# Performance work log

Hardware: AMD Instinct MI355X
Metric: run time of the kernel (lower is better)

Reference implementation:

```python
import jax, jax.numpy as jnp
import numpy as np

B, N, F_IN = 8, 4096, 32
NRP = 1024
D_MODEL = 512
K = 64  # max_num_neighbors
STAGE_CFG = ((1024, 0.05), (256, 0.3), (64, 0.5))  # (num_samples=ceil(0.25*N_in), radius)


def fps(pos, m):
    """Farthest point sampling of m points from pos (N,3), deterministic start at 0."""
    d = jnp.sum((pos - pos[0]) ** 2, axis=-1)
    idxs = jnp.zeros((m,), jnp.int32)
    def body(i, carry):
        idxs, d = carry
        nxt = jnp.argmax(d).astype(jnp.int32)
        d = jnp.minimum(d, jnp.sum((pos - pos[nxt]) ** 2, axis=-1))
        return (idxs.at[i].set(nxt), d)
    idxs, _ = jax.lax.fori_loop(1, m, body, (idxs, d))
    return idxs


def apply_mlp(h, ws, bs):
    for w, b in zip(ws[:-1], bs[:-1]):
        h = jax.nn.relu(h @ w + b)
    return h @ ws[-1] + bs[-1]


def sa_stage(x, pos, m, r, ws, bs):
    """SAModule: FPS -> radius neighbors (<=K) -> PointNetConv (gather, MLP, max-scatter)."""
    idx = jax.vmap(lambda p: fps(p, m))(pos)                          # (B,m)
    pos_s = jnp.take_along_axis(pos, idx[..., None], axis=1)          # (B,m,3)
    d2 = jnp.sum((pos_s[:, :, None, :] - pos[:, None, :, :]) ** 2, -1)  # (B,m,N)
    neg = jnp.where(d2 <= r * r, -d2, -jnp.inf)
    vals, nbr = jax.lax.top_k(neg, K)                                 # (B,m,K) nearest within r
    valid = vals > -jnp.inf                                           # self always valid (d2=0)
    x_j = jax.vmap(lambda xb, nb: xb[nb])(x, nbr)                     # (B,m,K,F) gather
    p_j = jax.vmap(lambda pb, nb: pb[nb])(pos, nbr)                   # (B,m,K,3)
    h = jnp.concatenate([x_j, p_j - pos_s[:, :, None, :]], axis=-1)   # message input
    h = apply_mlp(h, ws, bs)
    h = jnp.where(valid[..., None], h, -jnp.inf)
    return jnp.max(h, axis=2), pos_s                                  # max aggregation


def _forward(point_cloud_features, point_cloud, emb_table, point_id_emb, stage_params):
    x = emb_table[point_cloud_features[..., 0]]                       # (B,N,F_IN)
    x = x.at[:, :NRP].add(point_id_emb)
    pos = point_cloud
    for (m, r), (ws, bs) in zip(STAGE_CFG, stage_params):
        x, pos = sa_stage(x, pos, m, r, ws, bs)
    return x, pos                                                     # (B,64,D_MODEL), (B,64,3)


def setup_inputs() -> dict:
    key = jax.random.key(0)
    ks = iter(jax.random.split(key, 64))
    def nrm(shape, s=0.05):
        return s * jax.random.normal(next(ks), shape, dtype=jnp.float32)
    inp = {
        "point_cloud_features": jax.random.randint(next(ks), (B, N, 1), 0, 3),
        "point_cloud": jax.random.uniform(next(ks), (B, N, 3), dtype=jnp.float32),
        "emb_table": nrm((3, F_IN), 1.0),
        "point_id_emb": nrm((1, NRP, F_IN), 1.0),
    }
    dims = {"s1": [3 + F_IN, 64, 64, 64], "s2": [64 + 3, 128, 128, 256], "s3": [256 + 3, 256, 512, D_MODEL]}
    for s, d in dims.items():
        for i in range(3):
            inp[f"{s}w{i}"] = nrm((d[i], d[i + 1]))
            inp[f"{s}b{i}"] = jnp.zeros((d[i + 1],), jnp.float32)
    return inp


def reference(point_cloud_features, point_cloud, emb_table, point_id_emb,
              s1w0, s1b0, s1w1, s1b1, s1w2, s1b2,
              s2w0, s2b0, s2w1, s2b1, s2w2, s2b2,
              s3w0, s3b0, s3w1, s3b1, s3w2, s3b2):
    stage_params = [
        ([s1w0, s1w1, s1w2], [s1b0, s1b1, s1b2]),
        ([s2w0, s2w1, s2w2], [s2b0, s2b1, s2b2]),
        ([s3w0, s3w1, s3w2], [s3b0, s3b1, s3b2]),
    ]
    return _forward(point_cloud_features, point_cloud, emb_table, point_id_emb, stage_params)
```

## Files before the change

kernel.cpp:

```cpp
#include <hip/hip_runtime.h>

#define DEVI static __device__ __forceinline__

constexpr int B = 8;
constexpr int N0 = 4096;
constexpr int KNB = 64;

typedef float f32x2 __attribute__((ext_vector_type(2)));
typedef float f32x4 __attribute__((ext_vector_type(4)));
typedef short bf16x8 __attribute__((ext_vector_type(8)));

DEVI float dist2f(float ax, float ay, float az, float bx, float by, float bz) {
#pragma clang fp contract(off)
  float dx = ax - bx;
  float dy = ay - by;
  float dz = az - bz;
  return (dx * dx + dy * dy) + dz * dz;
}
DEVI f32x2 dist2v(f32x2 ax, f32x2 ay, f32x2 az, float bx, float by, float bz) {
#pragma clang fp contract(off)
  f32x2 dx = ax - bx;
  f32x2 dy = ay - by;
  f32x2 dz = az - bz;
  return (dx * dx + dy * dy) + dz * dz;
}

DEVI unsigned long long packMinKey(float v, int i) {
  return ((unsigned long long)__float_as_uint(v) << 32) | (unsigned int)i;
}

template <int CTRL, int RM>
DEVI unsigned long long dppMaxU64(unsigned long long k) {
  unsigned lo = (unsigned)k, hi = (unsigned)(k >> 32);
  unsigned mlo = (unsigned)__builtin_amdgcn_update_dpp((int)lo, (int)lo, CTRL, RM, 0xf, false);
  unsigned mhi = (unsigned)__builtin_amdgcn_update_dpp((int)hi, (int)hi, CTRL, RM, 0xf, false);
  unsigned long long o = ((unsigned long long)mhi << 32) | mlo;
  return (k > o) ? k : o;
}
DEVI unsigned long long waveReduceMaxU64(unsigned long long k) {
  k = dppMaxU64<0x111, 0xf>(k);
  k = dppMaxU64<0x112, 0xf>(k);
  k = dppMaxU64<0x114, 0xf>(k);
  k = dppMaxU64<0x118, 0xf>(k);
  k = dppMaxU64<0x142, 0xa>(k);
  k = dppMaxU64<0x143, 0xc>(k);
  unsigned lo = (unsigned)__builtin_amdgcn_readlane((int)(unsigned)k, 63);
  unsigned hi = (unsigned)__builtin_amdgcn_readlane((int)(unsigned)(k >> 32), 63);
  return ((unsigned long long)hi << 32) | lo;
}

DEVI unsigned short bfhi(float x) {
  unsigned u = __float_as_uint(x);
  return (unsigned short)((u + 0x7FFFu + ((u >> 16) & 1u)) >> 16);
}
DEVI float bf2f(unsigned short h) { return __uint_as_float(((unsigned)h) << 16); }
DEVI void mkfrag(const float* p, bf16x8& hi, bf16x8& lo) {
#pragma unroll
  for (int e = 0; e < 8; ++e) {
    float x = p[e];
    unsigned short h = bfhi(x);
    float r = x - bf2f(h);
    unsigned short l2 = bfhi(r);
    hi[e] = (short)h;
    lo[e] = (short)l2;
  }
}


DEVI void x0_body(const int* __restrict__ feat, const float* __restrict__ emb,
                  const float* __restrict__ pid, float* __restrict__ x0buf,
                  int bx, int t) {
  int gid = bx * 256 + t;
  if (gid >= B * N0 * 32) return;
  int c = gid & 31;
  int bn = gid >> 5;
  int n = bn & (N0 - 1);
  int f = feat[bn];
  float v = emb[f * 32 + c];
  if (n < 1024) v += pid[n * 32 + c];
  x0buf[gid] = v;
}

DEVI void pack_body(int gid, const float* __restrict__ W, int Kreal, int KS,
                    int N, unsigned short* __restrict__ hi,
                    unsigned short* __restrict__ lo) {
  int e = gid & 7;
  int l = (gid >> 3) & 63;
  int rest = gid >> 9;
  int ks = rest % KS;
  int nt = rest / KS;
  int n = nt * 16 + (l & 15);
  int k = ks * 32 + (l >> 4) * 8 + e;
  float val = (k < Kreal) ? W[(size_t)k * N + n] : 0.f;
  unsigned short h = bfhi(val);
  float r = val - bf2f(h);
  hi[gid] = h;
  lo[gid] = bfhi(r);
}

template <int NPTS, int M, int BLK>
DEVI void fps_body(char* smem, const float* __restrict__ pos,
                   float* __restrict__ pos_out, int b, int t) {
  constexpr int EPT = NPTS / BLK;
  constexpr int EP2 = EPT / 2;
  constexpr int NW = BLK / 64;
  float4* posl = (float4*)smem;
  float4* outp = (float4*)(smem + (size_t)NPTS * 16);
  unsigned long long* redk =
      (unsigned long long*)(smem + (size_t)(NPTS + M) * 16);
  const float* pb = pos + (size_t)b * NPTS * 3;
  f32x2 px[EP2], py[EP2], pz[EP2], d[EP2];
#pragma unroll
  for (int e = 0; e < EP2; ++e) {
    int i0 = t + (2 * e) * BLK;
    int i1 = t + (2 * e + 1) * BLK;
    float x0 = pb[i0 * 3 + 0], y0 = pb[i0 * 3 + 1], z0 = pb[i0 * 3 + 2];
    float x1 = pb[i1 * 3 + 0], y1 = pb[i1 * 3 + 1], z1 = pb[i1 * 3 + 2];
    px[e] = (f32x2){x0, x1};
    py[e] = (f32x2){y0, y1};
    pz[e] = (f32x2){z0, z1};
    posl[i0] = make_float4(x0, y0, z0, 0.f);
    posl[i1] = make_float4(x1, y1, z1, 0.f);
  }
  float sx = pb[0], sy = pb[1], sz = pb[2];
  if (t == 0) outp[0] = make_float4(sx, sy, sz, 0.f);
  f32x2 m2 = (f32x2){-1.f, -1.f};
#pragma unroll
  for (int e = 0; e < EP2; ++e) {
    d[e] = dist2v(px[e], py[e], pz[e], sx, sy, sz);
    m2.x = fmaxf(m2.x, d[e].x);
    m2.y = fmaxf(m2.y, d[e].y);
  }
  for (int it = 1; it < M; ++it) {
    const float lm = fmaxf(m2.x, m2.y);
    unsigned cand = 0xffffffffu;
#pragma unroll
    for (int e = 0; e < EP2; ++e) {
      unsigned c0 = (d[e].x == lm) ? (unsigned)(t + (2 * e) * BLK) : 0xffffffffu;
      unsigned c1 = (d[e].y == lm) ? (unsigned)(t + (2 * e + 1) * BLK) : 0xffffffffu;
      unsigned cc = c0 < c1 ? c0 : c1;
      cand = cand < cc ? cand : cc;
    }
    unsigned long long k =
        ((unsigned long long)__float_as_uint(lm) << 32) |
        (unsigned)(0x7fffffffu - cand);
    k = waveReduceMaxU64(k);
    unsigned sel;
    if constexpr (NW > 1) {
      if ((t & 63) == 0) redk[(it & 1) * NW + (t >> 6)] = k;
      __syncthreads();
      unsigned long long kk = redk[(it & 1) * NW + 0];
#pragma unroll
      for (int w = 1; w < NW; ++w) {
        unsigned long long o = redk[(it & 1) * NW + w];
        kk = (kk > o) ? kk : o;
      }
      sel = 0x7fffffffu - (unsigned)(kk & 0xffffffffULL);
    } else {
      sel = 0x7fffffffu - (unsigned)(k & 0xffffffffULL);
    }
    float4 sp = posl[sel];
    if (t == 0) outp[it] = sp;
    f32x2 mm = (f32x2){-1.f, -1.f};
#pragma unroll
    for (int e = 0; e < EP2; ++e) {
      f32x2 nd = dist2v(px[e], py[e], pz[e], sp.x, sp.y, sp.z);
      d[e].x = fminf(d[e].x, nd.x);
      d[e].y = fminf(d[e].y, nd.y);
      mm.x = fmaxf(mm.x, d[e].x);
      mm.y = fmaxf(mm.y, d[e].y);
    }
    m2 = mm;
  }
  if constexpr (NW > 1) __syncthreads();
  for (int m = t; m < M; m += BLK) {
    float4 q = outp[m];
    pos_out[(size_t)(b * M + m) * 3 + 0] = q.x;
    pos_out[(size_t)(b * M + m) * 3 + 1] = q.y;
    pos_out[(size_t)(b * M + m) * 3 + 2] = q.z;
  }
}

template <int NPTS, int M>
DEVI void radius_body(char* smem, const float* __restrict__ pos,
                      const float* __restrict__ pos_s, float r2,
                      int* __restrict__ nbr, int* __restrict__ cnt, int blk,
                      int t) {
  unsigned long long* candkey = (unsigned long long*)smem;
  int* ctrp = (int*)(smem + (size_t)NPTS * 8);
  const int b = blk / M;
  const float* pb = pos + (size_t)b * NPTS * 3;
  const float cx = pos_s[(size_t)blk * 3 + 0];
  const float cy = pos_s[(size_t)blk * 3 + 1];
  const float cz = pos_s[(size_t)blk * 3 + 2];
  if (t == 0) *ctrp = 0;
  __syncthreads();
  for (int j = t; j < NPTS; j += 256) {
    float d2 = dist2f(pb[j * 3 + 0], pb[j * 3 + 1], pb[j * 3 + 2], cx, cy, cz);
    if (d2 <= r2) {
      int p = atomicAdd(ctrp, 1);
      candkey[p] = packMinKey(d2, j);
      if (p < KNB) nbr[(size_t)blk * KNB + p] = j;
    }
  }
  __syncthreads();
  const int c = *ctrp;
  if (c <= KNB) {
    if (t == 0) cnt[blk] = c;
    return;
  }
  for (int s = t; s < c; s += 256) {
    unsigned long long mykey = candkey[s];
    int rank = 0;
#pragma unroll 4
    for (int j = 0; j < c; ++j) {
      rank += (candkey[j] < mykey) ? 1 : 0;
    }
    if (rank < KNB)
      nbr[(size_t)blk * KNB + rank] = (int)(unsigned)(mykey & 0xffffffffULL);
  }
  if (t == 0) cnt[blk] = KNB;
}

DEVI void conv1_body(char* smem, const float* __restrict__ x0buf,
                     const float* __restrict__ pos,
                     const float* __restrict__ pos_s,
                     const int* __restrict__ nbr, const int* __restrict__ cntp,
                     const float* __restrict__ w0, const float* __restrict__ b0,
                     const float* __restrict__ w1, const float* __restrict__ b1,
                     const float* __restrict__ w2, const float* __restrict__ b2,
                     float* __restrict__ x1, int blk, int t) {
  float(*ins)[36] = (float(*)[36])smem;
  float(*hh)[65] = (float(*)[65])(smem + 576);
  float(*sred)[65] = (float(*)[65])(smem + 1616);
  const int slot = t >> 6;
  const int ch = t & 63;
  const int b = blk >> 10;
  const int c = cntp[blk];
  const float cx = pos_s[(size_t)blk * 3 + 0];
  const float cy = pos_s[(size_t)blk * 3 + 1];
  const float cz = pos_s[(size_t)blk * 3 + 2];
  float best = -__builtin_inff();
  for (int r0 = 0; r0 < c; r0 += 4) {
    const int r = r0 + slot;
    const bool act = r < c;
    const int j = nbr[(size_t)blk * KNB + (act ? r : 0)];
    if (ch < 32) {
      ins[slot][ch] = x0buf[((size_t)(b * N0) + j) * 32 + ch];
    } else if (ch < 35) {
      float pv = pos[((size_t)(b * N0) + j) * 3 + (ch - 32)];
      float cv = (ch == 32) ? cx : (ch == 33) ? cy : cz;
      ins[slot][ch] = pv - cv;
    }
    __syncthreads();
    float v = b0[ch];
#pragma unroll
    for (int i = 0; i < 35; ++i) v = fmaf(ins[slot][i], w0[i * 64 + ch], v);
    v = fmaxf(v, 0.f);
    hh[slot][ch] = v;
    __syncthreads();
    float v2 = b1[ch];
#pragma unroll
    for (int i = 0; i < 64; ++i) v2 = fmaf(hh[slot][i], w1[i * 64 + ch], v2);
    v2 = fmaxf(v2, 0.f);
    __syncthreads();
    hh[slot][ch] = v2;
    __syncthreads();
    float v3 = b2[ch];
#pragma unroll
    for (int i = 0; i < 64; ++i) v3 = fmaf(hh[slot][i], w2[i * 64 + ch], v3);
    if (act) best = fmaxf(best, v3);
    __syncthreads();
  }
  sred[slot][ch] = best;
  __syncthreads();
  if (t < 64) {
    float v = sred[0][t];
#pragma unroll
    for (int s = 1; s < 4; ++s) v = fmaxf(v, sred[s][t]);
    x1[(size_t)blk * 64 + t] = v;
  }
}

DEVI void conv2_mfma_body(char* smem, const float* __restrict__ x1,
                          const float* __restrict__ pos1,
                          const float* __restrict__ pos2,
                          const int* __restrict__ nbr,
                          const int* __restrict__ cntp,
                          const unsigned short* __restrict__ w0h,
                          const float* __restrict__ b0,
                          const unsigned short* __restrict__ w1h,
                          const float* __restrict__ b1,
                          const unsigned short* __restrict__ w2h,
                          const float* __restrict__ b2,
                          float* __restrict__ x2, int blk, int t) {
  float(*h1)[132] = (float(*)[132])smem;
  float(*h2)[132] = (float(*)[132])(smem + 33792);
  float* red = (float*)smem;
  const int b = blk >> 8;
  const int c = cntp[blk];
  const int w = t >> 6;
  const int lane = t & 63;
  const int cb = lane & 15;
  const int kb = lane >> 4;
  const int mrow = w * 16 + cb;
  const int jrow = nbr[(size_t)blk * KNB + (mrow < c ? mrow : c - 1)];
  const float* xrow = x1 + ((size_t)(b * 1024) + jrow) * 64;
  const float cx = pos2[(size_t)blk * 3 + 0];
  const float cy = pos2[(size_t)blk * 3 + 1];
  const float cz = pos2[(size_t)blk * 3 + 2];

  f32x4 acc1[8];
#pragma unroll
  for (int nt = 0; nt < 8; ++nt) acc1[nt] = (f32x4){0.f, 0.f, 0.f, 0.f};
#pragma unroll
  for (int ks = 0; ks < 2; ++ks) {
    float xv[8];
    *(float4*)&xv[0] = *(const float4*)&xrow[ks * 32 + kb * 8];
    *(float4*)&xv[4] = *(const float4*)&xrow[ks * 32 + kb * 8 + 4];
    bf16x8 ahi, alo;
    mkfrag(xv, ahi, alo);
#pragma unroll
    for (int nt = 0; nt < 8; ++nt) {
      size_t off = ((size_t)(nt * 3 + ks) * 64 + lane) * 8;
      bf16x8 bhi = *(const bf16x8*)(w0h + off);
      acc1[nt] = __builtin_amdgcn_mfma_f32_16x16x32_bf16(ahi, bhi, acc1[nt], 0, 0, 0);
      acc1[nt] = __builtin_amdgcn_mfma_f32_16x16x32_bf16(alo, bhi, acc1[nt], 0, 0, 0);
    }
  }
  {
    float xv[8] = {0.f, 0.f, 0.f, 0.f, 0.f, 0.f, 0.f, 0.f};
    if (kb == 0) {
      xv[0] = pos1[((size_t)(b * 1024) + jrow) * 3 + 0] - cx;
      xv[1] = pos1[((size_t)(b * 1024) + jrow) * 3 + 1] - cy;
      xv[2] = pos1[((size_t)(b * 1024) + jrow) * 3 + 2] - cz;
    }
    bf16x8 ahi, alo;
    mkfrag(xv, ahi, alo);
#pragma unroll
    for (int nt = 0; nt < 8; ++nt) {
      size_t off = ((size_t)(nt * 3 + 2) * 64 + lane) * 8;
      bf16x8 bhi = *(const bf16x8*)(w0h + off);
      acc1[nt] = __builtin_amdgcn_mfma_f32_16x16x32_bf16(ahi, bhi, acc1[nt], 0, 0, 0);
      acc1[nt] = __builtin_amdgcn_mfma_f32_16x16x32_bf16(alo, bhi, acc1[nt], 0, 0, 0);
    }
  }
  {
    const int mw = w * 16 + kb * 4;
#pragma unroll
    for (int nt = 0; nt < 8; ++nt) {
      float bias = b0[nt * 16 + cb];
#pragma unroll
      for (int r = 0; r < 4; ++r)
        h1[mw + r][nt * 16 + cb] = fmaxf(acc1[nt][r] + bias, 0.f);
    }
  }

  f32x4 acc2[8];
#pragma unroll
  for (int nt = 0; nt < 8; ++nt) acc2[nt] = (f32x4){0.f, 0.f, 0.f, 0.f};
#pragma unroll
  for (int ks = 0; ks < 4; ++ks) {
    bf16x8 ahi, alo;
    mkfrag(&h1[mrow][ks * 32 + kb * 8], ahi, alo);
#pragma unroll
    for (int nt = 0; nt < 8; ++nt) {
      size_t off = ((size_t)(nt * 4 + ks) * 64 + lane) * 8;
      bf16x8 bhi = *(const bf16x8*)(w1h + off);
      acc2[nt] = __builtin_amdgcn_mfma_f32_16x16x32_bf16(ahi, bhi, acc2[nt], 0, 0, 0);
      acc2[nt] = __builtin_amdgcn_mfma_f32_16x16x32_bf16(alo, bhi, acc2[nt], 0, 0, 0);
    }
  }
  {
    const int mw = w * 16 + kb * 4;
#pragma unroll
    for (int nt = 0; nt < 8; ++nt) {
      float bias = b1[nt * 16 + cb];
#pragma unroll
      for (int r = 0; r < 4; ++r)
        h2[mw + r][nt * 16 + cb] = fmaxf(acc2[nt][r] + bias, 0.f);
    }
  }

  f32x4 acc3[16];
#pragma unroll
  for (int nt = 0; nt < 16; ++nt) acc3[nt] = (f32x4){0.f, 0.f, 0.f, 0.f};
#pragma unroll
  for (int ks = 0; ks < 4; ++ks) {
    bf16x8 ahi, alo;
    mkfrag(&h2[mrow][ks * 32 + kb * 8], ahi, alo);
#pragma unroll
    for (int nt = 0; nt < 16; ++nt) {
      size_t off = ((size_t)(nt * 4 + ks) * 64 + lane) * 8;
      bf16x8 bhi = *(const bf16x8*)(w2h + off);
      acc3[nt] = __builtin_amdgcn_mfma_f32_16x16x32_bf16(ahi, bhi, acc3[nt], 0, 0, 0);
      acc3[nt] = __builtin_amdgcn_mfma_f32_16x16x32_bf16(alo, bhi, acc3[nt], 0, 0, 0);
    }
  }
  __syncthreads();
  {
    const int mw = w * 16 + kb * 4;
#pragma unroll
    for (int nt = 0; nt < 16; ++nt) {
      float bias = b2[nt * 16 + cb];
      float mx = -__builtin_inff();
#pragma unroll
      for (int r = 0; r < 4; ++r) {
        if (mw + r < c) mx = fmaxf(mx, acc3[nt][r] + bias);
      }
      red[(w * 4 + kb) * 256 + nt * 16 + cb] = mx;
    }
  }
  __syncthreads();
  {
    float v = red[t];
#pragma unroll
    for (int g = 1; g < 16; ++g) v = fmaxf(v, red[g * 256 + t]);
    x2[(size_t)blk * 256 + t] = v;
  }
}


constexpr int PK_T0 = 16 * 9 * 64 * 8;
constexpr int PK_T1 = 32 * 8 * 64 * 8;
constexpr int PK_T2 = 32 * 16 * 64 * 8;
constexpr int PK_U0 = 8 * 3 * 64 * 8;
constexpr int PK_U1 = 8 * 4 * 64 * 8;
constexpr int PK_U2 = 16 * 4 * 64 * 8;
constexpr int PK_TOTAL = PK_T0 + PK_T1 + PK_T2 + PK_U0 + PK_U1 + PK_U2;
constexpr int PK_BLOCKS = PK_TOTAL / 256;

__global__ void __launch_bounds__(256) l1_kernel(
    const float* __restrict__ pos, float* __restrict__ pos1,
    const int* __restrict__ feat, const float* __restrict__ emb,
    const float* __restrict__ pid, float* __restrict__ x0buf,
    const float* __restrict__ s3w0, const float* __restrict__ s3w1,
    const float* __restrict__ s3w2, const float* __restrict__ s2w0,
    const float* __restrict__ s2w1, const float* __restrict__ s2w2,
    unsigned short* __restrict__ w0h, unsigned short* __restrict__ w0l,
    unsigned short* __restrict__ w1h, unsigned short* __restrict__ w1l,
    unsigned short* __restrict__ w2h, unsigned short* __restrict__ w2l,
    unsigned short* __restrict__ v0h, unsigned short* __restrict__ v0l,
    unsigned short* __restrict__ v1h, unsigned short* __restrict__ v1l,
    unsigned short* __restrict__ v2h, unsigned short* __restrict__ v2l) {
  __shared__ __attribute__((aligned(16))) char smem[81984];
  int bx = blockIdx.x;
  if (bx < 8) {
    fps_body<4096, 1024, 256>(smem, pos, pos1, bx, threadIdx.x);
    return;
  }
  bx -= 8;
  if (bx < 4096) {
    x0_body(feat, emb, pid, x0buf, bx, threadIdx.x);
    return;
  }
  bx -= 4096;
  int gid = bx * 256 + threadIdx.x;
  if (gid < PK_T0) { pack_body(gid, s3w0, 259, 9, 256, w0h, w0l); return; }
  gid -= PK_T0;
  if (gid < PK_T1) { pack_body(gid, s3w1, 256, 8, 512, w1h, w1l); return; }
  gid -= PK_T1;
  if (gid < PK_T2) { pack_body(gid, s3w2, 512, 16, 512, w2h, w2l); return; }
  gid -= PK_T2;
  if (gid < PK_U0) { pack_body(gid, s2w0, 67, 3, 128, v0h, v0l); return; }
  gid -= PK_U0;
  if (gid < PK_U1) { pack_body(gid, s2w1, 128, 4, 128, v1h, v1l); return; }
  gid -= PK_U1;
  if (gid < PK_U2) { pack_body(gid, s2w2, 128, 4, 256, v2h, v2l); return; }
}

__global__ void __launch_bounds__(256) l2_kernel(
    const float* __restrict__ pos1, float* __restrict__ pos2,
    const float* __restrict__ pos, float r2a, int* __restrict__ nbr1,
    int* __restrict__ cnt1) {
  __shared__ __attribute__((aligned(16))) char smem[33024];
  if (blockIdx.x < 8) {
    if (threadIdx.x < 64)
      fps_body<1024, 256, 64>(smem, pos1, pos2, blockIdx.x, threadIdx.x);
  } else {
    radius_body<4096, 1024>(smem, pos, pos1, r2a, nbr1, cnt1, blockIdx.x - 8,
                            threadIdx.x);
  }
}

__global__ void __launch_bounds__(256) l3_kernel(
    const float* __restrict__ pos2, float* __restrict__ pos3, float r2b,
    int* __restrict__ nbr2, int* __restrict__ cnt2,
    const float* __restrict__ pos1, const float* __restrict__ x0buf,
    const float* __restrict__ pos, const int* __restrict__ nbr1,
    const int* __restrict__ cnt1, const float* __restrict__ w0,
    const float* __restrict__ b0, const float* __restrict__ w1,
    const float* __restrict__ b1, const float* __restrict__ w2,
    const float* __restrict__ b2, float* __restrict__ x1) {
  __shared__ __attribute__((aligned(16))) char smem[8448];
  if (blockIdx.x < 8) {
    if (threadIdx.x < 64)
      fps_body<256, 64, 64>(smem, pos2, pos3, blockIdx.x, threadIdx.x);
  } else if (blockIdx.x < 8 + 2048) {
    radius_body<1024, 256>(smem, pos1, pos2, r2b, nbr2, cnt2, blockIdx.x - 8,
                           threadIdx.x);
  } else {
    conv1_body(smem, x0buf, pos, pos1, nbr1, cnt1, w0, b0, w1, b1, w2, b2, x1,
               blockIdx.x - (8 + 2048), threadIdx.x);
  }
}

__global__ void __launch_bounds__(256) l4_kernel(
    const float* __restrict__ pos2, const float* __restrict__ pos3, float r2c,
    int* __restrict__ nbr3, int* __restrict__ cnt3,
    const float* __restrict__ x1, const float* __restrict__ pos1,
    const int* __restrict__ nbr2, const int* __restrict__ cnt2,
    const unsigned short* __restrict__ v0h, const float* __restrict__ b0,
    const unsigned short* __restrict__ v1h, const float* __restrict__ b1,
    const unsigned short* __restrict__ v2h, const float* __restrict__ b2,
    float* __restrict__ x2) {
  __shared__ __attribute__((aligned(16))) char smem[67584];
  if (blockIdx.x < 512) {
    radius_body<256, 64>(smem, pos2, pos3, r2c, nbr3, cnt3, blockIdx.x,
                         threadIdx.x);
  } else {
    conv2_mfma_body(smem, x1, pos1, pos2, nbr2, cnt2, v0h, b0, v1h, b1, v2h,
                    b2, x2, blockIdx.x - 512, threadIdx.x);
  }
}

__global__ void __launch_bounds__(256) conv3_mfma(
    const float* __restrict__ x2, const float* __restrict__ pos2,
    const float* __restrict__ pos3, const int* __restrict__ nbr,
    const int* __restrict__ cntp,
    const unsigned short* __restrict__ w0h, const float* __restrict__ b0,
    const unsigned short* __restrict__ w1h, const float* __restrict__ b1,
    const unsigned short* __restrict__ w2h, const float* __restrict__ b2,
    float* __restrict__ out) {
  __shared__ __attribute__((aligned(16))) float h1s[64 * 268];
  __shared__ __attribute__((aligned(16))) float h2cs[64 * 140];
  const int blk = blockIdx.x;
  const int t = threadIdx.x;
  const int b = blk >> 6;
  const int c = cntp[blk];
  const int w = t >> 6;
  const int lane = t & 63;
  const int cb = lane & 15;
  const int kb = lane >> 4;
  const float cx = pos3[(size_t)blk * 3 + 0];
  const float cy = pos3[(size_t)blk * 3 + 1];
  const float cz = pos3[(size_t)blk * 3 + 2];
  const int mrow = w * 16 + cb;
  const int jrow = nbr[(size_t)blk * KNB + (mrow < c ? mrow : c - 1)];
  const float* xrow = x2 + ((size_t)(b * 256) + jrow) * 256;

  f32x4 acc1[16];
#pragma unroll
  for (int nt = 0; nt < 16; ++nt) acc1[nt] = (f32x4){0.f, 0.f, 0.f, 0.f};
#pragma unroll
  for (int ks = 0; ks < 8; ++ks) {
    float xv[8];
    *(float4*)&xv[0] = *(const float4*)&xrow[ks * 32 + kb * 8];
    *(float4*)&xv[4] = *(const float4*)&xrow[ks * 32 + kb * 8 + 4];
    bf16x8 ahi, alo;
    mkfrag(xv, ahi, alo);
#pragma unroll
    for (int nt = 0; nt < 16; ++nt) {
      size_t off = ((size_t)(nt * 9 + ks) * 64 + lane) * 8;
      bf16x8 bhi = *(const bf16x8*)(w0h + off);
      acc1[nt] = __builtin_amdgcn_mfma_f32_16x16x32_bf16(ahi, bhi, acc1[nt], 0, 0, 0);
      acc1[nt] = __builtin_amdgcn_mfma_f32_16x16x32_bf16(alo, bhi, acc1[nt], 0, 0, 0);
    }
  }
  {
    float xv[8] = {0.f, 0.f, 0.f, 0.f, 0.f, 0.f, 0.f, 0.f};
    if (kb == 0) {
      xv[0] = pos2[((size_t)(b * 256) + jrow) * 3 + 0] - cx;
      xv[1] = pos2[((size_t)(b * 256) + jrow) * 3 + 1] - cy;
      xv[2] = pos2[((size_t)(b * 256) + jrow) * 3 + 2] - cz;
    }
    bf16x8 ahi, alo;
    mkfrag(xv, ahi, alo);
#pragma unroll
    for (int nt = 0; nt < 16; ++nt) {
      size_t off = ((size_t)(nt * 9 + 8) * 64 + lane) * 8;
      bf16x8 bhi = *(const bf16x8*)(w0h + off);
      acc1[nt] = __builtin_amdgcn_mfma_f32_16x16x32_bf16(ahi, bhi, acc1[nt], 0, 0, 0);
      acc1[nt] = __builtin_amdgcn_mfma_f32_16x16x32_bf16(alo, bhi, acc1[nt], 0, 0, 0);
    }
  }
  {
    const int mw = w * 16 + kb * 4;
#pragma unroll
    for (int nt = 0; nt < 16; ++nt) {
      float bias = b0[nt * 16 + cb];
#pragma unroll
      for (int r = 0; r < 4; ++r)
        h1s[(mw + r) * 268 + nt * 16 + cb] = fmaxf(acc1[nt][r] + bias, 0.f);
    }
  }

  f32x4 acc3[32];
#pragma unroll
  for (int nt = 0; nt < 32; ++nt) acc3[nt] = (f32x4){0.f, 0.f, 0.f, 0.f};
  for (int ch = 0; ch < 4; ++ch) {
    f32x4 acc2[8];
#pragma unroll
    for (int nt = 0; nt < 8; ++nt) acc2[nt] = (f32x4){0.f, 0.f, 0.f, 0.f};
#pragma unroll
    for (int ks = 0; ks < 8; ++ks) {
      bf16x8 ahi, alo;
      mkfrag(&h1s[mrow * 268 + ks * 32 + kb * 8], ahi, alo);
#pragma unroll
      for (int nt = 0; nt < 8; ++nt) {
        size_t off = ((size_t)((ch * 8 + nt) * 8 + ks) * 64 + lane) * 8;
        bf16x8 bhi = *(const bf16x8*)(w1h + off);
        acc2[nt] = __builtin_amdgcn_mfma_f32_16x16x32_bf16(ahi, bhi, acc2[nt], 0, 0, 0);
        acc2[nt] = __builtin_amdgcn_mfma_f32_16x16x32_bf16(alo, bhi, acc2[nt], 0, 0, 0);
      }
    }
    {
      const int mw = w * 16 + kb * 4;
#pragma unroll
      for (int nt = 0; nt < 8; ++nt) {
        float bias = b1[ch * 128 + nt * 16 + cb];
#pragma unroll
        for (int r = 0; r < 4; ++r)
          h2cs[(mw + r) * 140 + nt * 16 + cb] = fmaxf(acc2[nt][r] + bias, 0.f);
      }
    }
#pragma unroll
    for (int ks3 = 0; ks3 < 4; ++ks3) {
      bf16x8 ahi, alo;
      mkfrag(&h2cs[mrow * 140 + ks3 * 32 + kb * 8], ahi, alo);
#pragma unroll
      for (int nt = 0; nt < 32; ++nt) {
        size_t off = ((size_t)(nt * 16 + ch * 4 + ks3) * 64 + lane) * 8;
        bf16x8 bhi = *(const bf16x8*)(w2h + off);
        acc3[nt] = __builtin_amdgcn_mfma_f32_16x16x32_bf16(ahi, bhi, acc3[nt], 0, 0, 0);
        acc3[nt] = __builtin_amdgcn_mfma_f32_16x16x32_bf16(alo, bhi, acc3[nt], 0, 0, 0);
      }
    }
  }

  __syncthreads();
  float* redw = h1s;
  {
    const int mw = w * 16 + kb * 4;
#pragma unroll
    for (int nt = 0; nt < 32; ++nt) {
      float bias = b2[nt * 16 + cb];
      float mx = -__builtin_inff();
#pragma unroll
      for (int r = 0; r < 4; ++r) {
        if (mw + r < c) mx = fmaxf(mx, acc3[nt][r] + bias);
      }
      redw[(w * 4 + kb) * 512 + nt * 16 + cb] = mx;
    }
  }
  __syncthreads();
#pragma unroll
  for (int half = 0; half < 2; ++half) {
    int col = t + half * 256;
    float v = redw[col];
#pragma unroll
    for (int g = 1; g < 16; ++g) v = fmaxf(v, redw[g * 512 + col]);
    out[(size_t)blk * 512 + col] = v;
  }
}

extern "C" void kernel_launch(void* const* d_in, const int* in_sizes, int n_in,
                              void* d_out, int out_size, void* d_ws, size_t ws_size,
                              hipStream_t stream) {
  const int* feat = (const int*)d_in[0];
  const float* pos = (const float*)d_in[1];
  const float* emb = (const float*)d_in[2];
  const float* pid = (const float*)d_in[3];
  const float* s1w0 = (const float*)d_in[4];
  const float* s1b0 = (const float*)d_in[5];
  const float* s1w1 = (const float*)d_in[6];
  const float* s1b1 = (const float*)d_in[7];
  const float* s1w2 = (const float*)d_in[8];
  const float* s1b2 = (const float*)d_in[9];
  const float* s2w0 = (const float*)d_in[10];
  const float* s2b0 = (const float*)d_in[11];
  const float* s2w1 = (const float*)d_in[12];
  const float* s2b1 = (const float*)d_in[13];
  const float* s2w2 = (const float*)d_in[14];
  const float* s2b2 = (const float*)d_in[15];
  const float* s3w0 = (const float*)d_in[16];
  const float* s3b0 = (const float*)d_in[17];
  const float* s3w1 = (const float*)d_in[18];
  const float* s3b1 = (const float*)d_in[19];
  const float* s3w2 = (const float*)d_in[20];
  const float* s3b2 = (const float*)d_in[21];
  (void)in_sizes; (void)n_in; (void)out_size; (void)ws_size;

  char* ws = (char*)d_ws;
  size_t off = 0;
  auto alloc = [&](size_t nbytes) {
    void* p = ws + off;
    off = (off + nbytes + 255) & ~(size_t)255;
    return p;
  };
  float* x0 = (float*)alloc((size_t)B * N0 * 32 * 4);
  float* pos1 = (float*)alloc((size_t)B * 1024 * 3 * 4);
  int* nbr1 = (int*)alloc((size_t)B * 1024 * KNB * 4);
  int* cnt1 = (int*)alloc((size_t)B * 1024 * 4);
  float* x1 = (float*)alloc((size_t)B * 1024 * 64 * 4);
  float* pos2 = (float*)alloc((size_t)B * 256 * 3 * 4);
  int* nbr2 = (int*)alloc((size_t)B * 256 * KNB * 4);
  int* cnt2 = (int*)alloc((size_t)B * 256 * 4);
  float* x2 = (float*)alloc((size_t)B * 256 * 256 * 4);
  int* nbr3 = (int*)alloc((size_t)B * 64 * KNB * 4);
  int* cnt3 = (int*)alloc((size_t)B * 64 * 4);
  unsigned short* w0h = (unsigned short*)alloc((size_t)PK_T0 * 2);
  unsigned short* w0l = (unsigned short*)alloc((size_t)PK_T0 * 2);
  unsigned short* w1h = (unsigned short*)alloc((size_t)PK_T1 * 2);
  unsigned short* w1l = (unsigned short*)alloc((size_t)PK_T1 * 2);
  unsigned short* w2h = (unsigned short*)alloc((size_t)PK_T2 * 2);
  unsigned short* w2l = (unsigned short*)alloc((size_t)PK_T2 * 2);
  unsigned short* v0h = (unsigned short*)alloc((size_t)PK_U0 * 2);
  unsigned short* v0l = (unsigned short*)alloc((size_t)PK_U0 * 2);
  unsigned short* v1h = (unsigned short*)alloc((size_t)PK_U1 * 2);
  unsigned short* v1l = (unsigned short*)alloc((size_t)PK_U1 * 2);
  unsigned short* v2h = (unsigned short*)alloc((size_t)PK_U2 * 2);
  unsigned short* v2l = (unsigned short*)alloc((size_t)PK_U2 * 2);

  float* xout = (float*)d_out;
  float* pos3 = xout + (size_t)B * 64 * 512;

  const float r2a = (float)(0.05 * 0.05);
  const float r2b = (float)(0.3 * 0.3);
  const float r2c = (float)(0.5 * 0.5);

  l1_kernel<<<8 + 4096 + PK_BLOCKS, 256, 0, stream>>>(
      pos, pos1, feat, emb, pid, x0, s3w0, s3w1, s3w2, s2w0, s2w1, s2w2,
      w0h, w0l, w1h, w1l, w2h, w2l, v0h, v0l, v1h, v1l, v2h, v2l);
  l2_kernel<<<8 + 8192, 256, 0, stream>>>(pos1, pos2, pos, r2a, nbr1, cnt1);
  l3_kernel<<<8 + 2048 + 8192, 256, 0, stream>>>(
      pos2, pos3, r2b, nbr2, cnt2, pos1, x0, pos, nbr1, cnt1,
      s1w0, s1b0, s1w1, s1b1, s1w2, s1b2, x1);
  l4_kernel<<<512 + 2048, 256, 0, stream>>>(
      pos2, pos3, r2c, nbr3, cnt3, x1, pos1, nbr2, cnt2,
      v0h, s2b0, v1h, s2b1, v2h, s2b2, x2);
  conv3_mfma<<<B * 64, 256, 0, stream>>>(x2, pos2, pos3, nbr3, cnt3,
                                         w0h, s3b0, w1h, s3b1, w2h, s3b2, xout);
}
```

Baseline: 1.248 ms.

## Merge four stage kernels into one dataflow megakernel with global flag sync

Replaces the four sequential layer kernels with a single persistent-style kernel whose blocks are ordered by stage and use global atomic flags and counters to wait on their exact producers. Radius search and convolution for one batch can then start as soon as that batch's FPS finishes, overlapping the serial FPS chain with the rest of the work instead of waiting at kernel boundaries. FPS now writes sampled positions directly to global memory on each iteration rather than staging them in shared memory. The risks are spin-wait occupancy (waiting blocks hold CU slots), reliance on blocks being dispatched in index order to avoid deadlock, an extra memset, and larger shared memory for all blocks reducing occupancy for the small ones.

```diff
diff --git a/kernel.cpp b/kernel.cpp
--- a/kernel.cpp
+++ b/kernel.cpp
@@ -64,6 +64,21 @@
     hi[e] = (short)h;
     lo[e] = (short)l2;
   }
+}
+
+DEVI void waitFlag(int* f) {
+  while (__hip_atomic_load(f, __ATOMIC_ACQUIRE, __HIP_MEMORY_SCOPE_AGENT) == 0)
+    __builtin_amdgcn_s_sleep(8);
+}
+DEVI void waitCount(int* f, int target) {
+  while (__hip_atomic_load(f, __ATOMIC_ACQUIRE, __HIP_MEMORY_SCOPE_AGENT) < target)
+    __builtin_amdgcn_s_sleep(8);
+}
+DEVI void setFlag(int* f) {
+  __hip_atomic_store(f, 1, __ATOMIC_RELEASE, __HIP_MEMORY_SCOPE_AGENT);
+}
+DEVI void bumpCount(int* f) {
+  __hip_atomic_fetch_add(f, 1, __ATOMIC_RELEASE, __HIP_MEMORY_SCOPE_AGENT);
 }
 
 
@@ -105,9 +120,8 @@
   constexpr int EP2 = EPT / 2;
   constexpr int NW = BLK / 64;
   float4* posl = (float4*)smem;
-  float4* outp = (float4*)(smem + (size_t)NPTS * 16);
   unsigned long long* redk =
-      (unsigned long long*)(smem + (size_t)(NPTS + M) * 16);
+      (unsigned long long*)(smem + (size_t)NPTS * 16);
   const float* pb = pos + (size_t)b * NPTS * 3;
   f32x2 px[EP2], py[EP2], pz[EP2], d[EP2];
 #pragma unroll
@@ -123,7 +137,11 @@
     posl[i1] = make_float4(x1, y1, z1, 0.f);
   }
   float sx = pb[0], sy = pb[1], sz = pb[2];
-  if (t == 0) outp[0] = make_float4(sx, sy, sz, 0.f);
+  if (t == 0) {
+    pos_out[(size_t)(b * M) * 3 + 0] = sx;
+    pos_out[(size_t)(b * M) * 3 + 1] = sy;
+    pos_out[(size_t)(b * M) * 3 + 2] = sz;
+  }
   f32x2 m2 = (f32x2){-1.f, -1.f};
 #pragma unroll
   for (int e = 0; e < EP2; ++e) {
@@ -160,7 +178,11 @@
       sel = 0x7fffffffu - (unsigned)(k & 0xffffffffULL);
     }
     float4 sp = posl[sel];
-    if (t == 0) outp[it] = sp;
+    if (t == 0) {
+      pos_out[(size_t)(b * M + it) * 3 + 0] = sp.x;
+      pos_out[(size_t)(b * M + it) * 3 + 1] = sp.y;
+      pos_out[(size_t)(b * M + it) * 3 + 2] = sp.z;
+    }
     f32x2 mm = (f32x2){-1.f, -1.f};
 #pragma unroll
     for (int e = 0; e < EP2; ++e) {
@@ -171,13 +193,6 @@
       mm.y = fmaxf(mm.y, d[e].y);
     }
     m2 = mm;
-  }
-  if constexpr (NW > 1) __syncthreads();
-  for (int m = t; m < M; m += BLK) {
-    float4 q = outp[m];
-    pos_out[(size_t)(b * M + m) * 3 + 0] = q.x;
-    pos_out[(size_t)(b * M + m) * 3 + 1] = q.y;
-    pos_out[(size_t)(b * M + m) * 3 + 2] = q.z;
   }
 }
 
@@ -430,8 +445,32 @@
 constexpr int PK_TOTAL = PK_T0 + PK_T1 + PK_T2 + PK_U0 + PK_U1 + PK_U2;
 constexpr int PK_BLOCKS = PK_TOTAL / 256;
 
-__global__ void __launch_bounds__(256) l1_kernel(
+constexpr int FL_F1 = 0;
+constexpr int FL_F2 = 8;
+constexpr int FL_F3 = 16;
+constexpr int FL_CX0 = 24;
+constexpr int FL_CPK = 25;
+constexpr int FL_CC1 = 26;
+constexpr int FL_R1 = 28;
+constexpr int FL_R2 = 28 + 8192;
+constexpr int FL_TOTAL = 28 + 8192 + 2048;
+
+constexpr int MG_FPS1 = 0;
+constexpr int MG_X0 = MG_FPS1 + 8;
+constexpr int MG_PACK = MG_X0 + 4096;
+constexpr int MG_FPS2 = MG_PACK + PK_BLOCKS;
+constexpr int MG_RAD1 = MG_FPS2 + 8;
+constexpr int MG_CONV1 = MG_RAD1 + 8192;
+constexpr int MG_FPS3 = MG_CONV1 + 8192;
+constexpr int MG_RAD2 = MG_FPS3 + 8;
+constexpr int MG_RAD3 = MG_RAD2 + 2048;
+constexpr int MG_CONV2 = MG_RAD3 + 512;
+constexpr int MG_TOTAL = MG_CONV2 + 2048;
+
+__global__ void __launch_bounds__(256) mega_kernel(
+    int* __restrict__ fl,
     const float* __restrict__ pos, float* __restrict__ pos1,
+    float* __restrict__ pos2, float* __restrict__ pos3,
     const int* __restrict__ feat, const float* __restrict__ emb,
     const float* __restrict__ pid, float* __restrict__ x0buf,
     const float* __restrict__ s3w0, const float* __restrict__ s3w1,
@@ -442,85 +481,111 @@
     unsigned short* __restrict__ w2h, unsigned short* __restrict__ w2l,
     unsigned short* __restrict__ v0h, unsigned short* __restrict__ v0l,
     unsigned short* __restrict__ v1h, unsigned short* __restrict__ v1l,
-    unsigned short* __restrict__ v2h, unsigned short* __restrict__ v2l) {
-  __shared__ __attribute__((aligned(16))) char smem[81984];
+    unsigned short* __restrict__ v2h, unsigned short* __restrict__ v2l,
+    float r2a, float r2b, float r2c,
+    int* __restrict__ nbr1, int* __restrict__ cnt1,
+    int* __restrict__ nbr2, int* __restrict__ cnt2,
+    int* __restrict__ nbr3, int* __restrict__ cnt3,
+    const float* __restrict__ s1w0, const float* __restrict__ s1b0,
+    const float* __restrict__ s1w1, const float* __restrict__ s1b1,
+    const float* __restrict__ s1w2, const float* __restrict__ s1b2,
+    float* __restrict__ x1,
+    const float* __restrict__ s2b0, const float* __restrict__ s2b1,
+    const float* __restrict__ s2b2, float* __restrict__ x2) {
+  __shared__ __attribute__((aligned(16))) char smem[67584];
+  const int t = threadIdx.x;
   int bx = blockIdx.x;
-  if (bx < 8) {
-    fps_body<4096, 1024, 256>(smem, pos, pos1, bx, threadIdx.x);
-    return;
-  }
-  bx -= 8;
-  if (bx < 4096) {
-    x0_body(feat, emb, pid, x0buf, bx, threadIdx.x);
-    return;
-  }
-  bx -= 4096;
-  int gid = bx * 256 + threadIdx.x;
-  if (gid < PK_T0) { pack_body(gid, s3w0, 259, 9, 256, w0h, w0l); return; }
-  gid -= PK_T0;
-  if (gid < PK_T1) { pack_body(gid, s3w1, 256, 8, 512, w1h, w1l); return; }
-  gid -= PK_T1;
-  if (gid < PK_T2) { pack_body(gid, s3w2, 512, 16, 512, w2h, w2l); return; }
-  gid -= PK_T2;
-  if (gid < PK_U0) { pack_body(gid, s2w0, 67, 3, 128, v0h, v0l); return; }
-  gid -= PK_U0;
-  if (gid < PK_U1) { pack_body(gid, s2w1, 128, 4, 128, v1h, v1l); return; }
-  gid -= PK_U1;
-  if (gid < PK_U2) { pack_body(gid, s2w2, 128, 4, 256, v2h, v2l); return; }
-}
-
-__global__ void __launch_bounds__(256) l2_kernel(
-    const float* __restrict__ pos1, float* __restrict__ pos2,
-    const float* __restrict__ pos, float r2a, int* __restrict__ nbr1,
-    int* __restrict__ cnt1) {
-  __shared__ __attribute__((aligned(16))) char smem[33024];
-  if (blockIdx.x < 8) {
-    if (threadIdx.x < 64)
-      fps_body<1024, 256, 64>(smem, pos1, pos2, blockIdx.x, threadIdx.x);
-  } else {
-    radius_body<4096, 1024>(smem, pos, pos1, r2a, nbr1, cnt1, blockIdx.x - 8,
-                            threadIdx.x);
-  }
-}
-
-__global__ void __launch_bounds__(256) l3_kernel(
-    const float* __restrict__ pos2, float* __restrict__ pos3, float r2b,
-    int* __restrict__ nbr2, int* __restrict__ cnt2,
-    const float* __restrict__ pos1, const float* __restrict__ x0buf,
-    const float* __restrict__ pos, const int* __restrict__ nbr1,
-    const int* __restrict__ cnt1, const float* __restrict__ w0,
-    const float* __restrict__ b0, const float* __restrict__ w1,
-    const float* __restrict__ b1, const float* __restrict__ w2,
-    const float* __restrict__ b2, float* __restrict__ x1) {
-  __shared__ __attribute__((aligned(16))) char smem[8448];
-  if (blockIdx.x < 8) {
-    if (threadIdx.x < 64)
-      fps_body<256, 64, 64>(smem, pos2, pos3, blockIdx.x, threadIdx.x);
-  } else if (blockIdx.x < 8 + 2048) {
-    radius_body<1024, 256>(smem, pos1, pos2, r2b, nbr2, cnt2, blockIdx.x - 8,
-                           threadIdx.x);
-  } else {
-    conv1_body(smem, x0buf, pos, pos1, nbr1, cnt1, w0, b0, w1, b1, w2, b2, x1,
-               blockIdx.x - (8 + 2048), threadIdx.x);
-  }
-}
-
-__global__ void __launch_bounds__(256) l4_kernel(
-    const float* __restrict__ pos2, const float* __restrict__ pos3, float r2c,
-    int* __restrict__ nbr3, int* __restrict__ cnt3,
-    const float* __restrict__ x1, const float* __restrict__ pos1,
-    const int* __restrict__ nbr2, const int* __restrict__ cnt2,
-    const unsigned short* __restrict__ v0h, const float* __restrict__ b0,
-    const unsigned short* __restrict__ v1h, const float* __restrict__ b1,
-    const unsigned short* __restrict__ v2h, const float* __restrict__ b2,
-    float* __restrict__ x2) {
-  __shared__ __attribute__((aligned(16))) char smem[67584];
-  if (blockIdx.x < 512) {
-    radius_body<256, 64>(smem, pos2, pos3, r2c, nbr3, cnt3, blockIdx.x,
-                         threadIdx.x);
-  } else {
-    conv2_mfma_body(smem, x1, pos1, pos2, nbr2, cnt2, v0h, b0, v1h, b1, v2h,
-                    b2, x2, blockIdx.x - 512, threadIdx.x);
+  if (bx < MG_X0) {
+    fps_body<4096, 1024, 256>(smem, pos, pos1, bx, t);
+    __syncthreads();
+    if (t == 0) setFlag(fl + FL_F1 + bx);
+    return;
+  }
+  if (bx < MG_PACK) {
+    x0_body(feat, emb, pid, x0buf, bx - MG_X0, t);
+    __syncthreads();
+    if (t == 0) bumpCount(fl + FL_CX0);
+    return;
+  }
+  if (bx < MG_FPS2) {
+    int gid = (bx - MG_PACK) * 256 + t;
+    if (gid < PK_T0) { pack_body(gid, s3w0, 259, 9, 256, w0h, w0l); }
+    else if ((gid -= PK_T0) < PK_T1) { pack_body(gid, s3w1, 256, 8, 512, w1h, w1l); }
+    else if ((gid -= PK_T1) < PK_T2) { pack_body(gid, s3w2, 512, 16, 512, w2h, w2l); }
+    else if ((gid -= PK_T2) < PK_U0) { pack_body(gid, s2w0, 67, 3, 128, v0h, v0l); }
+    else if ((gid -= PK_U0) < PK_U1) { pack_body(gid, s2w1, 128, 4, 128, v1h, v1l); }
+    else { pack_body(gid - PK_U1, s2w2, 128, 4, 256, v2h, v2l); }
+    __syncthreads();
+    if (t == 0) bumpCount(fl + FL_CPK);
+    return;
+  }
+  if (bx < MG_RAD1) {
+    int b = bx - MG_FPS2;
+    if (t == 0) waitFlag(fl + FL_F1 + b);
+    __syncthreads();
+    if (t < 64) fps_body<1024, 256, 64>(smem, pos1, pos2, b, t);
+    __syncthreads();
+    if (t == 0) setFlag(fl + FL_F2 + b);
+    return;
+  }
+  if (bx < MG_CONV1) {
+    int i = bx - MG_RAD1;
+    if (t == 0) waitFlag(fl + FL_F1 + (i >> 10));
+    __syncthreads();
+    radius_body<4096, 1024>(smem, pos, pos1, r2a, nbr1, cnt1, i, t);
+    __syncthreads();
+    if (t == 0) setFlag(fl + FL_R1 + i);
+    return;
+  }
+  if (bx < MG_FPS3) {
+    int i = bx - MG_CONV1;
+    if (t == 0) {
+      waitFlag(fl + FL_R1 + i);
+      waitCount(fl + FL_CX0, 4096);
+    }
+    __syncthreads();
+    conv1_body(smem, x0buf, pos, pos1, nbr1, cnt1, s1w0, s1b0, s1w1, s1b1,
+               s1w2, s1b2, x1, i, t);
+    __syncthreads();
+    if (t == 0) bumpCount(fl + FL_CC1);
+    return;
+  }
+  if (bx < MG_RAD2) {
+    int b = bx - MG_FPS3;
+    if (t == 0) waitFlag(fl + FL_F2 + b);
+    __syncthreads();
+    if (t < 64) fps_body<256, 64, 64>(smem, pos2, pos3, b, t);
+    __syncthreads();
+    if (t == 0) setFlag(fl + FL_F3 + b);
+    return;
+  }
+  if (bx < MG_RAD3) {
+    int i = bx - MG_RAD2;
+    if (t == 0) waitFlag(fl + FL_F2 + (i >> 8));
+    __syncthreads();
+    radius_body<1024, 256>(smem, pos1, pos2, r2b, nbr2, cnt2, i, t);
+    __syncthreads();
+    if (t == 0) setFlag(fl + FL_R2 + i);
+    return;
+  }
+  if (bx < MG_CONV2) {
+    int i = bx - MG_RAD3;
+    if (t == 0) waitFlag(fl + FL_F3 + (i >> 6));
+    __syncthreads();
+    radius_body<256, 64>(smem, pos2, pos3, r2c, nbr3, cnt3, i, t);
+    return;
+  }
+  {
+    int i = bx - MG_CONV2;
+    if (t == 0) {
+      waitFlag(fl + FL_R2 + i);
+      waitCount(fl + FL_CC1, 8192);
+      waitCount(fl + FL_CPK, PK_BLOCKS);
+    }
+    __syncthreads();
+    conv2_mfma_body(smem, x1, pos1, pos2, nbr2, cnt2, v0h, s2b0, v1h, s2b1,
+                    v2h, s2b2, x2, i, t);
+    return;
   }
 }
 
@@ -721,6 +786,7 @@
   unsigned short* v1l = (unsigned short*)alloc((size_t)PK_U1 * 2);
   unsigned short* v2h = (unsigned short*)alloc((size_t)PK_U2 * 2);
   unsigned short* v2l = (unsigned short*)alloc((size_t)PK_U2 * 2);
+  int* fl = (int*)alloc((size_t)FL_TOTAL * 4);
 
   float* xout = (float*)d_out;
   float* pos3 = xout + (size_t)B * 64 * 512;
@@ -729,16 +795,13 @@
   const float r2b = (float)(0.3 * 0.3);
   const float r2c = (float)(0.5 * 0.5);
 
-  l1_kernel<<<8 + 4096 + PK_BLOCKS, 256, 0, stream>>>(
-      pos, pos1, feat, emb, pid, x0, s3w0, s3w1, s3w2, s2w0, s2w1, s2w2,
-      w0h, w0l, w1h, w1l, w2h, w2l, v0h, v0l, v1h, v1l, v2h, v2l);
-  l2_kernel<<<8 + 8192, 256, 0, stream>>>(pos1, pos2, pos, r2a, nbr1, cnt1);
-  l3_kernel<<<8 + 2048 + 8192, 256, 0, stream>>>(
-      pos2, pos3, r2b, nbr2, cnt2, pos1, x0, pos, nbr1, cnt1,
-      s1w0, s1b0, s1w1, s1b1, s1w2, s1b2, x1);
-  l4_kernel<<<512 + 2048, 256, 0, stream>>>(
-      pos2, pos3, r2c, nbr3, cnt3, x1, pos1, nbr2, cnt2,
-      v0h, s2b0, v1h, s2b1, v2h, s2b2, x2);
+  hipMemsetAsync(fl, 0, (size_t)FL_TOTAL * 4, stream);
+  mega_kernel<<<MG_TOTAL, 256, 0, stream>>>(
+      fl, pos, pos1, pos2, pos3, feat, emb, pid, x0,
+      s3w0, s3w1, s3w2, s2w0, s2w1, s2w2,
+      w0h, w0l, w1h, w1l, w2h, w2l, v0h, v0l, v1h, v1l, v2h, v2l,
+      r2a, r2b, r2c, nbr1, cnt1, nbr2, cnt2, nbr3, cnt3,
+      s1w0, s1b0, s1w1, s1b1, s1w2, s1b2, x1, s2b0, s2b1, s2b2, x2);
   conv3_mfma<<<B * 64, 256, 0, stream>>>(x2, pos2, pos3, nbr3, cnt3,
                                          w0h, s3b0, w1h, s3b1, w2h, s3b2, xout);
 }
```

Result: slower. 1.744 ms (+39.8%).
